# Performance work log

Measured on AMD Instinct MI355X. Metric: run time of the kernel, lower is better.

## Reference

```python
import jax, jax.numpy as jnp
import numpy as np

H = 1024   # hidden_dim
B = 4096   # batch
T = 128    # forecast_len
IN = 1     # output_dim (univariate)


def setup_inputs() -> dict:
    key = jax.random.key(0)
    ks = jax.random.split(key, 8)
    s = 1.0 / np.sqrt(H)  # torch LSTM/Linear default uniform init scale
    u = lambda k, shape: jax.random.uniform(k, shape, jnp.float32, -s, s)
    return {
        "hidden": jax.random.normal(ks[0], (1, B, H), jnp.float32),
        "cell":   jax.random.normal(ks[1], (1, B, H), jnp.float32),
        "W_ih":   u(ks[2], (4 * H, IN)),   # torch gate order: i, f, g, o
        "W_hh":   u(ks[3], (4 * H, H)),
        "b_ih":   u(ks[4], (4 * H,)),
        "b_hh":   u(ks[5], (4 * H,)),
        "W_out":  u(ks[6], (IN, H)),
        "b_out":  u(ks[7], (IN,)),
    }


def reference(hidden, cell, W_ih, W_hh, b_ih, b_hh, W_out, b_out):
    h = hidden[0]  # [B, H]  (num_layers == 1)
    c = cell[0]    # [B, H]
    x0 = jnp.zeros((h.shape[0], IN), h.dtype)  # initial decoder input = zeros
    b = b_ih + b_hh

    def step(carry, _):
        x, h, c = carry
        gates = x @ W_ih.T + h @ W_hh.T + b          # [B, 4H]
        i, f, g, o = jnp.split(gates, 4, axis=-1)    # torch order i,f,g,o
        c = jax.nn.sigmoid(f) * c + jax.nn.sigmoid(i) * jnp.tanh(g)
        h = jax.nn.sigmoid(o) * jnp.tanh(c)
        pred = h @ W_out.T + b_out                   # [B, 1]
        return (pred, h, c), pred                    # prediction fed back as next input

    _, preds = jax.lax.scan(step, (x0, h, c), None, length=T)  # [T, B, 1]
    return jnp.transpose(preds, (1, 0, 2))  # [B, T, 1]
```

## Files before the change

### kernel.cpp

```cpp
#include <hip/hip_runtime.h>
#include <hip/hip_bf16.h>
#include <stdint.h>


#define HH 1024
#define BB 4096
#define TT 128

#define BM 128
#define BKK 64

typedef __bf16 bf16;
typedef __bf16 v8bf __attribute__((ext_vector_type(8)));
typedef float f32x4 __attribute__((ext_vector_type(4)));

__device__ __forceinline__ float fast_sigmoid(float x) {
    return 1.0f / (1.0f + __expf(-x));
}
__device__ __forceinline__ float fast_tanh(float x) {
    return 1.0f - 2.0f / (__expf(2.0f * x) + 1.0f);
}

__device__ __forceinline__ void gload_lds16(const void* g, void* l) {
    __builtin_amdgcn_global_load_lds(
        (const __attribute__((address_space(1))) uint32_t*)(uintptr_t)g,
        (__attribute__((address_space(3))) uint32_t*)(uint32_t)(uintptr_t)l,
        16, 0, 0);
}


__global__ void prep_weights(const float* __restrict__ Whh,
                             const float* __restrict__ bih,
                             const float* __restrict__ bhh,
                             bf16* __restrict__ Wr,
                             float* __restrict__ bias) {
    int idx = blockIdx.x * blockDim.x + threadIdx.x;
    if (idx < 4 * HH * HH) {
        int k   = idx & (HH - 1);
        int row = idx >> 10;
        int jb2 = row >> 8;
        int g   = (row >> 6) & 3;
        int jj  = row & 63;
        int srow = g * HH + jb2 * 64 + jj;
        Wr[idx] = (bf16)Whh[srow * HH + k];
    }
    if (idx < 4 * HH) bias[idx] = bih[idx] + bhh[idx];
}

__global__ void prep_h(const float* __restrict__ h0, bf16* __restrict__ hb) {
    int idx = blockIdx.x * blockDim.x + threadIdx.x;
    if (idx < BB * HH) hb[idx] = (bf16)h0[idx];
}

__global__ void prep_pred(float* __restrict__ predbuf, const float* __restrict__ b_out) {
    int idx = blockIdx.x * blockDim.x + threadIdx.x;
    if (idx < (TT + 1) * BB) predbuf[idx] = (idx < BB) ? 0.0f : b_out[0];
}


__global__ __launch_bounds__(256, 2)
void lstm_step(const bf16* __restrict__ hread, bf16* __restrict__ hwrite,
               const float* __restrict__ cin, float* __restrict__ cout,
               const bf16* __restrict__ Wr, const float* __restrict__ bias,
               const float* __restrict__ Wih, const float* __restrict__ Wout,
               const float* __restrict__ predbuf_r, float* __restrict__ predbuf_w) {
    __shared__ bf16 As[BM][BKK];
    __shared__ bf16 Bs[2 * BM][BKK];

    const int tid   = threadIdx.x;
    const int lane  = tid & 63;
    const int w     = tid >> 6;
    const int waveM = w >> 1, waveN = w & 1;
    const int quad  = lane >> 4, l15 = lane & 15;

    const int bid    = blockIdx.x;
    const int jb2    = (bid & 7) * 2 + ((bid >> 3) & 1);
    const int blockB = (bid >> 4) * BM;

    f32x4 acc[4][8];
#pragma unroll
    for (int mi = 0; mi < 4; mi++)
#pragma unroll
        for (int nt = 0; nt < 8; nt++) acc[mi][nt] = (f32x4){0.f, 0.f, 0.f, 0.f};

    const bf16* Asrc = hread + (size_t)blockB * HH;
    const bf16* Bsrc = Wr + (size_t)jb2 * 256 * HH;

    const int r8  = lane >> 3;
    const int gc  = (lane & 7) ^ r8;
    const int swr = l15 & 7;

    for (int k0 = 0; k0 < HH; k0 += BKK) {
#pragma unroll
        for (int c2 = 0; c2 < 4; c2++) {
            const int rowb = w * 32 + c2 * 8;
            gload_lds16(Asrc + (size_t)(rowb + r8) * HH + k0 + gc * 8, &As[rowb][0]);
        }
#pragma unroll
        for (int c2 = 0; c2 < 8; c2++) {
            const int rowb = w * 64 + c2 * 8;
            gload_lds16(Bsrc + (size_t)(rowb + r8) * HH + k0 + gc * 8, &Bs[rowb][0]);
        }
        asm volatile("s_waitcnt vmcnt(0)" ::: "memory");
        __syncthreads();
#pragma unroll
        for (int kk = 0; kk < 2; kk++) {
            v8bf a[4], b[8];
            const int pch = ((kk * 4 + quad) ^ swr) * 8;
#pragma unroll
            for (int mi = 0; mi < 4; mi++)
                a[mi] = *(const v8bf*)&As[waveM * 64 + mi * 16 + l15][pch];
#pragma unroll
            for (int g = 0; g < 4; g++)
#pragma unroll
                for (int jh = 0; jh < 2; jh++)
                    b[g * 2 + jh] =
                        *(const v8bf*)&Bs[g * 64 + waveN * 32 + jh * 16 + l15][pch];
#pragma unroll
            for (int mi = 0; mi < 4; mi++)
#pragma unroll
                for (int nt = 0; nt < 8; nt++)
                    acc[mi][nt] = __builtin_amdgcn_mfma_f32_16x16x32_bf16(
                        a[mi], b[nt], acc[mi][nt], 0, 0, 0);
        }
        __syncthreads();
    }

    float wihv[2][4], bsvv[2][4], wov[2];
#pragma unroll
    for (int jh = 0; jh < 2; jh++) {
        const int j = jb2 * 64 + waveN * 32 + jh * 16 + l15;
#pragma unroll
        for (int g = 0; g < 4; g++) {
            wihv[jh][g] = Wih[g * HH + j];
            bsvv[jh][g] = bias[g * HH + j];
        }
        wov[jh] = Wout[j];
    }

#pragma unroll
    for (int mi = 0; mi < 4; mi++) {
#pragma unroll
        for (int r = 0; r < 4; r++) {
            const int b = blockB + waveM * 64 + mi * 16 + quad * 4 + r;
            const float x = predbuf_r[b];
            float pacc = 0.0f;
#pragma unroll
            for (int jh = 0; jh < 2; jh++) {
                const int j = jb2 * 64 + waveN * 32 + jh * 16 + l15;
                const float gi = acc[mi][0 + jh][r] + x * wihv[jh][0] + bsvv[jh][0];
                const float gf = acc[mi][2 + jh][r] + x * wihv[jh][1] + bsvv[jh][1];
                const float gg = acc[mi][4 + jh][r] + x * wihv[jh][2] + bsvv[jh][2];
                const float go = acc[mi][6 + jh][r] + x * wihv[jh][3] + bsvv[jh][3];
                const float cn = fast_sigmoid(gf) * cin[(size_t)b * HH + j]
                               + fast_sigmoid(gi) * fast_tanh(gg);
                cout[(size_t)b * HH + j] = cn;
                const float hn = fast_sigmoid(go) * fast_tanh(cn);
                hwrite[(size_t)b * HH + j] = (bf16)hn;
                pacc += hn * wov[jh];
            }
            pacc += __shfl_xor(pacc, 1);
            pacc += __shfl_xor(pacc, 2);
            pacc += __shfl_xor(pacc, 4);
            pacc += __shfl_xor(pacc, 8);
            if (l15 == 0) atomicAdd(&predbuf_w[b], pacc);
        }
    }
}


__global__ void write_out(const float* __restrict__ predbuf, float* __restrict__ out) {
    int idx = blockIdx.x * blockDim.x + threadIdx.x;
    if (idx < BB * TT) {
        int t = idx & (TT - 1);
        int b = idx >> 7;
        out[idx] = predbuf[(size_t)(t + 1) * BB + b];
    }
}


extern "C" void kernel_launch(void* const* d_in, const int* in_sizes, int n_in,
                              void* d_out, int out_size, void* d_ws, size_t ws_size,
                              hipStream_t stream) {
    const float* hidden = (const float*)d_in[0];
    const float* cell   = (const float*)d_in[1];
    const float* Wih    = (const float*)d_in[2];
    const float* Whh    = (const float*)d_in[3];
    const float* bih    = (const float*)d_in[4];
    const float* bhh    = (const float*)d_in[5];
    const float* Wout   = (const float*)d_in[6];
    const float* bout   = (const float*)d_in[7];
    float* out = (float*)d_out;

    char* ws = (char*)d_ws;
    bf16* Wr = (bf16*)ws;        ws += (size_t)4 * HH * HH * 2;
    bf16* hb0 = (bf16*)ws;       ws += (size_t)BB * HH * 2;
    bf16* hb1 = (bf16*)ws;       ws += (size_t)BB * HH * 2;
    float* cbuf = (float*)ws;    ws += (size_t)BB * HH * 4;
    float* bias = (float*)ws;    ws += (size_t)4 * HH * 4;
    float* predbuf = (float*)ws; ws += (size_t)(TT + 1) * BB * 4;

    prep_weights<<<(4 * HH * HH + 255) / 256, 256, 0, stream>>>(Whh, bih, bhh, Wr, bias);
    prep_h<<<(BB * HH + 255) / 256, 256, 0, stream>>>(hidden, hb0);
    prep_pred<<<((TT + 1) * BB + 255) / 256, 256, 0, stream>>>(predbuf, bout);

    bf16* hb[2] = {hb0, hb1};
    for (int t = 0; t < TT; t++) {
        const bf16* hr = hb[t & 1];
        bf16* hw = hb[(t + 1) & 1];
        const float* ci = (t == 0) ? cell : cbuf;
        lstm_step<<<16 * (BB / BM), 256, 0, stream>>>(
            hr, hw, ci, cbuf, Wr, bias, Wih, Wout,
            predbuf + (size_t)t * BB, predbuf + (size_t)(t + 1) * BB);
    }

    write_out<<<(BB * TT + 255) / 256, 256, 0, stream>>>(predbuf, out);
}
```

Before: 5.597 ms.

## Double-buffer weight tiles and prefetch next K-tile during MFMA compute

Restructures the K loop of the LSTM step GEMM so the next weight tile is loaded into a second LDS buffer while the current tile is multiplied. The A tile stays single-buffered: its fragments are read into registers first, a barrier follows, and then the next A tile is issued. The goal is to hide global-to-LDS latency behind MFMA work instead of stalling on vmcnt(0) before every tile. In exchange, LDS use rises by 32KB per block, which may cut occupancy from the two blocks per CU requested by launch_bounds, and more registers are live because of the full unroll and the held A fragments.

After: 5.754 ms. 2.8% more time.

```diff
diff --git a/kernel.cpp b/kernel.cpp
--- a/kernel.cpp
+++ b/kernel.cpp
@@ -9,6 +9,7 @@
 
 #define BM 128
 #define BKK 64
+#define NKT (HH / BKK)
 
 typedef __bf16 bf16;
 typedef __bf16 v8bf __attribute__((ext_vector_type(8)));
@@ -65,7 +66,7 @@
                const float* __restrict__ Wih, const float* __restrict__ Wout,
                const float* __restrict__ predbuf_r, float* __restrict__ predbuf_w) {
     __shared__ bf16 As[BM][BKK];
-    __shared__ bf16 Bs[2 * BM][BKK];
+    __shared__ bf16 Bs[2][2 * BM][BKK];
 
     const int tid   = threadIdx.x;
     const int lane  = tid & 63;
@@ -90,41 +91,68 @@
     const int gc  = (lane & 7) ^ r8;
     const int swr = l15 & 7;
 
-    for (int k0 = 0; k0 < HH; k0 += BKK) {
-#pragma unroll
-        for (int c2 = 0; c2 < 4; c2++) {
-            const int rowb = w * 32 + c2 * 8;
-            gload_lds16(Asrc + (size_t)(rowb + r8) * HH + k0 + gc * 8, &As[rowb][0]);
-        }
-#pragma unroll
-        for (int c2 = 0; c2 < 8; c2++) {
-            const int rowb = w * 64 + c2 * 8;
-            gload_lds16(Bsrc + (size_t)(rowb + r8) * HH + k0 + gc * 8, &Bs[rowb][0]);
-        }
-        asm volatile("s_waitcnt vmcnt(0)" ::: "memory");
-        __syncthreads();
+#define STAGE_A(k0)                                                           \
+    {                                                                         \
+        _Pragma("unroll")                                                     \
+        for (int c2 = 0; c2 < 4; c2++) {                                      \
+            const int rowb = w * 32 + c2 * 8;                                 \
+            gload_lds16(Asrc + (size_t)(rowb + r8) * HH + (k0) + gc * 8,      \
+                        &As[rowb][0]);                                        \
+        }                                                                     \
+    }
+#define STAGE_B(buf, k0)                                                      \
+    {                                                                         \
+        _Pragma("unroll")                                                     \
+        for (int c2 = 0; c2 < 8; c2++) {                                      \
+            const int rowb = w * 64 + c2 * 8;                                 \
+            gload_lds16(Bsrc + (size_t)(rowb + r8) * HH + (k0) + gc * 8,      \
+                        &Bs[buf][rowb][0]);                                   \
+        }                                                                     \
+    }
+
+    STAGE_A(0);
+    STAGE_B(0, 0);
+    asm volatile("s_waitcnt vmcnt(0)" ::: "memory");
+    __syncthreads();
+
+#pragma unroll
+    for (int kt = 0; kt < NKT; kt++) {
+        if (kt + 1 < NKT) STAGE_B((kt + 1) & 1, (kt + 1) * BKK);
+
+        v8bf a[2][4];
+#pragma unroll
+        for (int kk = 0; kk < 2; kk++)
+#pragma unroll
+            for (int mi = 0; mi < 4; mi++)
+                a[kk][mi] = *(const v8bf*)
+                    &As[waveM * 64 + mi * 16 + l15][((kk * 4 + quad) ^ swr) * 8];
+        asm volatile("s_waitcnt lgkmcnt(0)" ::: "memory");
+        asm volatile("s_barrier" ::: "memory");
+        if (kt + 1 < NKT) STAGE_A((kt + 1) * BKK);
+
 #pragma unroll
         for (int kk = 0; kk < 2; kk++) {
-            v8bf a[4], b[8];
+            v8bf b[8];
             const int pch = ((kk * 4 + quad) ^ swr) * 8;
 #pragma unroll
-            for (int mi = 0; mi < 4; mi++)
-                a[mi] = *(const v8bf*)&As[waveM * 64 + mi * 16 + l15][pch];
-#pragma unroll
             for (int g = 0; g < 4; g++)
 #pragma unroll
                 for (int jh = 0; jh < 2; jh++)
-                    b[g * 2 + jh] =
-                        *(const v8bf*)&Bs[g * 64 + waveN * 32 + jh * 16 + l15][pch];
+                    b[g * 2 + jh] = *(const v8bf*)
+                        &Bs[kt & 1][g * 64 + waveN * 32 + jh * 16 + l15][pch];
 #pragma unroll
             for (int mi = 0; mi < 4; mi++)
 #pragma unroll
                 for (int nt = 0; nt < 8; nt++)
                     acc[mi][nt] = __builtin_amdgcn_mfma_f32_16x16x32_bf16(
-                        a[mi], b[nt], acc[mi][nt], 0, 0, 0);
+                        a[kk][mi], b[nt], acc[mi][nt], 0, 0, 0);
         }
-        __syncthreads();
-    }
+
+        asm volatile("s_waitcnt vmcnt(0)" ::: "memory");
+        asm volatile("s_barrier" ::: "memory");
+    }
+#undef STAGE_A
+#undef STAGE_B
 
     float wihv[2][4], bsvv[2][4], wov[2];
 #pragma unroll
```

## Fold prediction feedback into recurrent weights and store cell state in bf16

Applied to the files above, without the earlier changes.

Since each step's input is W_out·h + b_out, W_ih·x is folded into a second bf16 copy of W_hh (W_hh + W_ih⊗W_out) and into the bias. This lets each step skip reading the previous prediction and the per-gate input FMAs. The bias now seeds the MFMA accumulators, and the cell state is held in a single in-place bf16 buffer instead of fp32, halving cell-state traffic. The trade-off is extra rounding: the folded weights are bf16, and the cell state is kept in bf16 across all 128 steps, which can accumulate error.

Result: faster. 5.344 ms (-4.5%).

```diff
diff --git a/kernel.cpp b/kernel.cpp
--- a/kernel.cpp
+++ b/kernel.cpp
@@ -32,8 +32,11 @@
 __global__ void prep_weights(const float* __restrict__ Whh,
                              const float* __restrict__ bih,
                              const float* __restrict__ bhh,
-                             bf16* __restrict__ Wr,
-                             float* __restrict__ bias) {
+                             const float* __restrict__ Wih,
+                             const float* __restrict__ Wout,
+                             const float* __restrict__ bout,
+                             bf16* __restrict__ Wr0, bf16* __restrict__ Wr1,
+                             float* __restrict__ bias0, float* __restrict__ bias1) {
     int idx = blockIdx.x * blockDim.x + threadIdx.x;
     if (idx < 4 * HH * HH) {
         int k   = idx & (HH - 1);
@@ -42,9 +45,15 @@
         int g   = (row >> 6) & 3;
         int jj  = row & 63;
         int srow = g * HH + jb2 * 64 + jj;
-        Wr[idx] = (bf16)Whh[srow * HH + k];
-    }
-    if (idx < 4 * HH) bias[idx] = bih[idx] + bhh[idx];
+        float wv = Whh[srow * HH + k];
+        Wr0[idx] = (bf16)wv;
+        Wr1[idx] = (bf16)(wv + Wih[srow] * Wout[k]);
+    }
+    if (idx < 4 * HH) {
+        float b = bih[idx] + bhh[idx];
+        bias0[idx] = b;
+        bias1[idx] = b + Wih[idx] * bout[0];
+    }
 }
 
 __global__ void prep_h(const float* __restrict__ h0, bf16* __restrict__ hb) {
@@ -52,18 +61,22 @@
     if (idx < BB * HH) hb[idx] = (bf16)h0[idx];
 }
 
+__global__ void prep_c(const float* __restrict__ c0, bf16* __restrict__ cb) {
+    int idx = blockIdx.x * blockDim.x + threadIdx.x;
+    if (idx < BB * HH) cb[idx] = (bf16)c0[idx];
+}
+
 __global__ void prep_pred(float* __restrict__ predbuf, const float* __restrict__ b_out) {
     int idx = blockIdx.x * blockDim.x + threadIdx.x;
-    if (idx < (TT + 1) * BB) predbuf[idx] = (idx < BB) ? 0.0f : b_out[0];
+    if (idx < (TT + 1) * BB) predbuf[idx] = b_out[0];
 }
 
 
 __global__ __launch_bounds__(256, 2)
 void lstm_step(const bf16* __restrict__ hread, bf16* __restrict__ hwrite,
-               const float* __restrict__ cin, float* __restrict__ cout,
-               const bf16* __restrict__ Wr, const float* __restrict__ bias,
-               const float* __restrict__ Wih, const float* __restrict__ Wout,
-               const float* __restrict__ predbuf_r, float* __restrict__ predbuf_w) {
+               bf16* __restrict__ cbuf,
+               const bf16* __restrict__ Wr, const float* __restrict__ biasp,
+               const float* __restrict__ Wout, float* __restrict__ predbuf_w) {
     __shared__ bf16 As[BM][BKK];
     __shared__ bf16 Bs[2 * BM][BKK];
 
@@ -77,12 +90,6 @@
     const int jb2    = (bid & 7) * 2 + ((bid >> 3) & 1);
     const int blockB = (bid >> 4) * BM;
 
-    f32x4 acc[4][8];
-#pragma unroll
-    for (int mi = 0; mi < 4; mi++)
-#pragma unroll
-        for (int nt = 0; nt < 8; nt++) acc[mi][nt] = (f32x4){0.f, 0.f, 0.f, 0.f};
-
     const bf16* Asrc = hread + (size_t)blockB * HH;
     const bf16* Bsrc = Wr + (size_t)jb2 * 256 * HH;
 
@@ -90,6 +97,26 @@
     const int gc  = (lane & 7) ^ r8;
     const int swr = l15 & 7;
 
+    float bsvv[2][4], wov[2];
+#pragma unroll
+    for (int jh = 0; jh < 2; jh++) {
+        const int j = jb2 * 64 + waveN * 32 + jh * 16 + l15;
+#pragma unroll
+        for (int g = 0; g < 4; g++) bsvv[jh][g] = biasp[g * HH + j];
+        wov[jh] = Wout[j];
+    }
+
+    f32x4 acc[4][8];
+#pragma unroll
+    for (int mi = 0; mi < 4; mi++)
+#pragma unroll
+        for (int g = 0; g < 4; g++)
+#pragma unroll
+            for (int jh = 0; jh < 2; jh++) {
+                const float bv = bsvv[jh][g];
+                acc[mi][g * 2 + jh] = (f32x4){bv, bv, bv, bv};
+            }
+
     for (int k0 = 0; k0 < HH; k0 += BKK) {
 #pragma unroll
         for (int c2 = 0; c2 < 4; c2++) {
@@ -126,35 +153,23 @@
         __syncthreads();
     }
 
-    float wihv[2][4], bsvv[2][4], wov[2];
-#pragma unroll
-    for (int jh = 0; jh < 2; jh++) {
-        const int j = jb2 * 64 + waveN * 32 + jh * 16 + l15;
-#pragma unroll
-        for (int g = 0; g < 4; g++) {
-            wihv[jh][g] = Wih[g * HH + j];
-            bsvv[jh][g] = bias[g * HH + j];
-        }
-        wov[jh] = Wout[j];
-    }
-
 #pragma unroll
     for (int mi = 0; mi < 4; mi++) {
 #pragma unroll
         for (int r = 0; r < 4; r++) {
             const int b = blockB + waveM * 64 + mi * 16 + quad * 4 + r;
-            const float x = predbuf_r[b];
             float pacc = 0.0f;
 #pragma unroll
             for (int jh = 0; jh < 2; jh++) {
                 const int j = jb2 * 64 + waveN * 32 + jh * 16 + l15;
-                const float gi = acc[mi][0 + jh][r] + x * wihv[jh][0] + bsvv[jh][0];
-                const float gf = acc[mi][2 + jh][r] + x * wihv[jh][1] + bsvv[jh][1];
-                const float gg = acc[mi][4 + jh][r] + x * wihv[jh][2] + bsvv[jh][2];
-                const float go = acc[mi][6 + jh][r] + x * wihv[jh][3] + bsvv[jh][3];
-                const float cn = fast_sigmoid(gf) * cin[(size_t)b * HH + j]
+                const float gi = acc[mi][0 + jh][r];
+                const float gf = acc[mi][2 + jh][r];
+                const float gg = acc[mi][4 + jh][r];
+                const float go = acc[mi][6 + jh][r];
+                const float cprev = (float)cbuf[(size_t)b * HH + j];
+                const float cn = fast_sigmoid(gf) * cprev
                                + fast_sigmoid(gi) * fast_tanh(gg);
-                cout[(size_t)b * HH + j] = cn;
+                cbuf[(size_t)b * HH + j] = (bf16)cn;
                 const float hn = fast_sigmoid(go) * fast_tanh(cn);
                 hwrite[(size_t)b * HH + j] = (bf16)hn;
                 pacc += hn * wov[jh];
@@ -193,25 +208,29 @@
     float* out = (float*)d_out;
 
     char* ws = (char*)d_ws;
-    bf16* Wr = (bf16*)ws;        ws += (size_t)4 * HH * HH * 2;
+    bf16* Wr0 = (bf16*)ws;       ws += (size_t)4 * HH * HH * 2;
+    bf16* Wr1 = (bf16*)ws;       ws += (size_t)4 * HH * HH * 2;
     bf16* hb0 = (bf16*)ws;       ws += (size_t)BB * HH * 2;
     bf16* hb1 = (bf16*)ws;       ws += (size_t)BB * HH * 2;
-    float* cbuf = (float*)ws;    ws += (size_t)BB * HH * 4;
-    float* bias = (float*)ws;    ws += (size_t)4 * HH * 4;
+    bf16* cbuf = (bf16*)ws;      ws += (size_t)BB * HH * 2;
+    float* bias0 = (float*)ws;   ws += (size_t)4 * HH * 4;
+    float* bias1 = (float*)ws;   ws += (size_t)4 * HH * 4;
     float* predbuf = (float*)ws; ws += (size_t)(TT + 1) * BB * 4;
 
-    prep_weights<<<(4 * HH * HH + 255) / 256, 256, 0, stream>>>(Whh, bih, bhh, Wr, bias);
+    prep_weights<<<(4 * HH * HH + 255) / 256, 256, 0, stream>>>(
+        Whh, bih, bhh, Wih, Wout, bout, Wr0, Wr1, bias0, bias1);
     prep_h<<<(BB * HH + 255) / 256, 256, 0, stream>>>(hidden, hb0);
+    prep_c<<<(BB * HH + 255) / 256, 256, 0, stream>>>(cell, cbuf);
     prep_pred<<<((TT + 1) * BB + 255) / 256, 256, 0, stream>>>(predbuf, bout);
 
     bf16* hb[2] = {hb0, hb1};
     for (int t = 0; t < TT; t++) {
         const bf16* hr = hb[t & 1];
         bf16* hw = hb[(t + 1) & 1];
-        const float* ci = (t == 0) ? cell : cbuf;
-        lstm_step<<<16 * (BB / BM), 256, 0, stream>>>(
-            hr, hw, ci, cbuf, Wr, bias, Wih, Wout,
-            predbuf + (size_t)t * BB, predbuf + (size_t)(t + 1) * BB);
+        const bf16* Wr   = (t == 0) ? Wr0 : Wr1;
+        const float* bsp = (t == 0) ? bias0 : bias1;
+        lstm_step<<<512, 256, 0, stream>>>(
+            hr, hw, cbuf, Wr, bsp, Wout, predbuf + (size_t)(t + 1) * BB);
     }
 
     write_out<<<(BB * TT + 255) / 256, 256, 0, stream>>>(predbuf, out);
```
